# Kernel tuning notes

Measured on AMD Instinct MI355X. Metric: run time of the kernel, lower is better.

## Reference

```python
import jax, jax.numpy as jnp
import numpy as np

NUM_E = 50000
EMBED_DIM = 128
HID_DIM = 200
B = 512
N = 50  # candidate_num / history length
ITER_NUM = 3
ALPHA = 0.5
WEIGHT_BASE = 1.0
SQUASH_W = 1.0
SQUASH_EPS = 1e-9
L2_EPS = 1e-12  # torch F.normalize default eps


def setup_inputs() -> dict:
    key = jax.random.key(0)
    k1, k2, k3, k4, k5, k6, k7 = jax.random.split(key, 7)
    idx = jax.random.randint(k1, (B, N), 0, NUM_E)
    times = jax.random.randint(k2, (B, N), 0, 365)
    # embeddings: normal then row-wise L2 normalize (as in init_embeddings)
    emb = jax.random.normal(k3, (NUM_E, EMBED_DIM), dtype=jnp.float32)
    embeddings = emb / jnp.maximum(jnp.linalg.norm(emb, axis=1, keepdims=True), L2_EPS)
    Ws_w = jax.random.normal(k4, (HID_DIM, EMBED_DIM), dtype=jnp.float32) * (2.0 / (HID_DIM + EMBED_DIM)) ** 0.5
    Ws_b = jnp.zeros((HID_DIM,), dtype=jnp.float32)
    mlp_w = jax.random.normal(k5, (NUM_E, HID_DIM), dtype=jnp.float32) * (2.0 / (NUM_E + HID_DIM)) ** 0.5
    mlp_b = jnp.zeros((NUM_E,), dtype=jnp.float32)
    return {"idx": idx, "times": times, "embeddings": embeddings,
            "Ws_w": Ws_w, "Ws_b": Ws_b, "mlp_w": mlp_w, "mlp_b": mlp_b}


def _squash(s):
    # s: [B, H]; squash over last axis (original axis=-2 on [B,1,1,H,1])
    sq = jnp.sum(s * s, axis=-1, keepdims=True)
    scale = sq / (SQUASH_W + sq) / jnp.sqrt(sq + SQUASH_EPS)
    return scale * s


def reference(idx, times, embeddings, Ws_w, Ws_b, mlp_w, mlp_b):
    # gather history embeddings: [B, N, D]
    embeds = embeddings[idx]
    # temporal weighting -> initial routing logits b_ij: [B, N]
    b = (WEIGHT_BASE + 1.0) / (WEIGHT_BASE + times.astype(jnp.float32))
    # Ws linear (dropout is identity at eval): [B, N, H]
    x = jnp.einsum('bnd,hd->bnh', embeds, Ws_w) + Ws_b
    # u_hat: L2-normalized over H
    u_hat = x / jnp.maximum(jnp.linalg.norm(x, axis=-1, keepdims=True), L2_EPS)
    u_det = jax.lax.stop_gradient(u_hat)
    # dynamic routing, fixed ITER_NUM iterations
    for r in range(ITER_NUM):
        c = jax.nn.softmax(b, axis=1) * N            # [B, N]
        s = jnp.einsum('bn,bnh->bh', c, u_hat)       # [B, H]
        v = _squash(s)                               # [B, H]
        if r < ITER_NUM - 1:
            b = b + jnp.einsum('bnh,bh->bn', u_det, v)
    poses, c_ij = v, c                               # [B, H], [B, N]
    # p_ij: scatter-add c_ij per entity id (math of one_hot^T @ c_ij)
    p = jnp.zeros((B, NUM_E), dtype=jnp.float32)
    p = p.at[jnp.arange(B)[:, None], idx].add(c_ij)
    p = jax.nn.softmax(p, axis=1)
    # decoder mlp (reflect=False)
    scores = poses @ mlp_w.T + mlp_b                 # [B, NUM_E]
    sims = jax.nn.softmax(scores, axis=1)
    return jnp.log(ALPHA * p + (1.0 - ALPHA) * sims)
```

## Files before the change

### kernel.cpp

```cpp
#include <hip/hip_runtime.h>
#include <stdint.h>

#define NUM_E 50000
#define EMBED_DIM 128
#define HID_DIM 200
#define BATCH 512
#define NN 50
#define KPAD 224
#define NKT 7
#define NTT2 3136
#define NXB 196
#define PACK_UNITS 784
#define USTRIDE 201

typedef short s16x8 __attribute__((ext_vector_type(8)));
typedef float f32x4 __attribute__((ext_vector_type(4)));

__device__ inline unsigned short f2bf(float f) {
  union { float f; unsigned u; } v; v.f = f;
  unsigned r = v.u + 0x7FFF + ((v.u >> 16) & 1);
  return (unsigned short)(r >> 16);
}
__device__ inline float bf2f(unsigned short b) {
  union { unsigned u; float f; } v; v.u = ((unsigned)b) << 16;
  return v.f;
}

__device__ __forceinline__ void gl_lds16(const unsigned short* g, unsigned short* l) {
  __builtin_amdgcn_global_load_lds(
      (const __attribute__((address_space(1))) unsigned int*)g,
      (__attribute__((address_space(3))) unsigned int*)l, 16, 0, 0);
}

__global__ __launch_bounds__(256, 4) void k_score(
    const unsigned short* __restrict__ Ap, const unsigned short* __restrict__ Bp,
    const float* __restrict__ mlp_b, unsigned short* __restrict__ stash,
    float* __restrict__ S_ws)
{
  __shared__ __align__(16) char buf[17408];
  const int id = blockIdx.x;
  const int yb = id / 200;
  const int xb = id - yb * 200;
  if (xb >= NXB) return;

  unsigned short* Bs = (unsigned short*)buf;
  float* red = (float*)(buf + 16384);
  const int tid = threadIdx.x;
  const int w = tid >> 6, lane = tid & 63;
  const int q = lane >> 4, l15 = lane & 15;
  const int mt0 = yb * 4;
  const int m0 = yb * 64;
  const int ntb = xb * 16 + w * 4;

  float bias[4];
  #pragma unroll
  for (int nl = 0; nl < 4; ++nl) {
    const int col = (ntb + nl) * 16 + l15;
    bias[nl] = (col < NUM_E) ? mlp_b[col] : 0.f;
  }
  const unsigned short* apBase = Ap + (size_t)mt0 * NKT * 512;

  f32x4 acc[4][4];
  #pragma unroll
  for (int i = 0; i < 4; i++)
    #pragma unroll
    for (int j = 0; j < 4; j++) acc[i][j] = (f32x4){0, 0, 0, 0};

  for (int kt = 0; kt < NKT; ++kt) {
    #pragma unroll
    for (int nl = 0; nl < 4; ++nl)
      gl_lds16(Bp + ((size_t)(ntb + nl) * NKT + kt) * 512 + lane * 8,
               &Bs[(w * 4 + nl) * 512]);
    s16x8 a[4];
    #pragma unroll
    for (int mi = 0; mi < 4; ++mi)
      a[mi] = *(const s16x8*)&apBase[((mi * NKT + kt) * 64 + lane) * 8];
    __syncthreads();
    s16x8 bfr[4];
    #pragma unroll
    for (int nl = 0; nl < 4; ++nl)
      bfr[nl] = *(const s16x8*)&Bs[((w * 4 + nl) * 64 + lane) * 8];
    #pragma unroll
    for (int nl = 0; nl < 4; ++nl)
      #pragma unroll
      for (int mi = 0; mi < 4; ++mi)
        acc[mi][nl] = __builtin_amdgcn_mfma_f32_16x16x32_bf16(a[mi], bfr[nl], acc[mi][nl], 0, 0, 0);
    __syncthreads();
  }

  float rs[4][4];
  #pragma unroll
  for (int mi = 0; mi < 4; mi++)
    #pragma unroll
    for (int p = 0; p < 4; p++) rs[mi][p] = 0.f;
  #pragma unroll
  for (int mi = 0; mi < 4; ++mi)
    #pragma unroll
    for (int nl = 0; nl < 4; ++nl) {
      const int col = (ntb + nl) * 16 + l15;
      #pragma unroll
      for (int p = 0; p < 4; p++) {
        if (col < NUM_E) {
          const float v = acc[mi][nl][p] + bias[nl];
          const unsigned short vb = f2bf(v);
          const int row = m0 + mi * 16 + q * 4 + p;
          stash[(size_t)row * NUM_E + col] = vb;
          rs[mi][p] += __expf(bf2f(vb));
        }
      }
    }
  #pragma unroll
  for (int m = 1; m < 16; m <<= 1)
    for (int mi = 0; mi < 4; mi++)
      for (int p = 0; p < 4; p++)
        rs[mi][p] += __shfl_xor(rs[mi][p], m, 64);
  if (l15 == 0)
    for (int mi = 0; mi < 4; mi++)
      for (int p = 0; p < 4; p++)
        red[w * 64 + mi * 16 + q * 4 + p] = rs[mi][p];
  __syncthreads();
  if (tid < 64)
    atomicAdd(&S_ws[m0 + tid],
              red[tid] + red[64 + tid] + red[128 + tid] + red[192 + tid]);
}

__global__ __launch_bounds__(256) void k_final(
    const unsigned short* __restrict__ stash,
    const float* __restrict__ D_ws, const float* __restrict__ S_ws,
    float* __restrict__ out)
{
  const int COLS8 = NUM_E / 8;
  const int total = BATCH * COLS8;
  const int stride = gridDim.x * 256;
  for (int u = blockIdx.x * 256 + threadIdx.x; u < total; u += stride) {
    const int b = u / COLS8;
    const int c8 = u - b * COLS8;
    const float invD = 0.5f / D_ws[b];
    const float invS = 0.5f / S_ws[b];
    const size_t base = (size_t)b * NUM_E + (size_t)c8 * 8;
    const uint4 raw = *(const uint4*)(stash + base);
    float o[8];
    const unsigned wds[4] = {raw.x, raw.y, raw.z, raw.w};
    #pragma unroll
    for (int j = 0; j < 4; ++j) {
      const float v0 = bf2f((unsigned short)(wds[j] & 0xFFFF));
      const float v1 = bf2f((unsigned short)(wds[j] >> 16));
      o[2 * j]     = __logf(fmaf(__expf(v0), invS, invD));
      o[2 * j + 1] = __logf(fmaf(__expf(v1), invS, invD));
    }
    *(float4*)(out + base)     = make_float4(o[0], o[1], o[2], o[3]);
    *(float4*)(out + base + 4) = make_float4(o[4], o[5], o[6], o[7]);
  }
}

__global__ __launch_bounds__(256, 3) void k_stage1(
    const int* __restrict__ idx, const int* __restrict__ times,
    const float* __restrict__ emb, const float* __restrict__ Ws_w,
    const float* __restrict__ Ws_b, const float* __restrict__ mlp_w,
    unsigned short* __restrict__ Bp, unsigned short* __restrict__ Ap,
    float* __restrict__ poses_f, float* __restrict__ expa_ws,
    float* __restrict__ D_ws, float* __restrict__ S_ws)
{
  __shared__ __align__(16) char buf[40320];
  __shared__ float cc[NN], bb[NN], vv[HID_DIM], red4[4], scaleS;
  __shared__ int sidx[NN];
  const int u = blockIdx.x;
  const int tid = threadIdx.x;
  const int w = tid >> 6, lane = tid & 63;
  const int q = lane >> 4, l15 = lane & 15;

  if (u < BATCH) {
    const int b = u;
    if (tid < NN) {
      sidx[tid] = idx[b * NN + tid];
      bb[tid] = 2.0f / (1.0f + (float)times[b * NN + tid]);
    }
    __syncthreads();
    unsigned short* Afr = (unsigned short*)buf;
    unsigned short* Bfr = (unsigned short*)(buf + 16384);
    for (int v = tid; v < 1024; v += 256) {
      const int row = v >> 4, c = v & 15;
      const int kt = c >> 2, qq = c & 3;
      unsigned short tmp[8] __attribute__((aligned(16)));
      if (row < NN) {
        const float* src = emb + (size_t)sidx[row] * EMBED_DIM + c * 8;
        float4 f0 = *(const float4*)src;
        float4 f1 = *(const float4*)(src + 4);
        tmp[0] = f2bf(f0.x); tmp[1] = f2bf(f0.y); tmp[2] = f2bf(f0.z); tmp[3] = f2bf(f0.w);
        tmp[4] = f2bf(f1.x); tmp[5] = f2bf(f1.y); tmp[6] = f2bf(f1.z); tmp[7] = f2bf(f1.w);
      } else {
        for (int j = 0; j < 8; j++) tmp[j] = 0;
      }
      *(uint4*)&Afr[(((row >> 4) * 4 + kt) * 64 + qq * 16 + (row & 15)) * 8] = *(uint4*)tmp;
    }
    f32x4 acc[4][4];
    #pragma unroll
    for (int i = 0; i < 4; i++)
      #pragma unroll
      for (int j = 0; j < 4; j++) acc[i][j] = (f32x4){0, 0, 0, 0};
    __syncthreads();
    for (int kt = 0; kt < 4; ++kt) {
      for (int v = tid; v < 832; v += 256) {
        const int n = v >> 2, cq = v & 3;
        unsigned short tmp[8] __attribute__((aligned(16)));
        if (n < HID_DIM) {
          const float* src = Ws_w + (size_t)n * EMBED_DIM + kt * 32 + cq * 8;
          float4 f0 = *(const float4*)src;
          float4 f1 = *(const float4*)(src + 4);
          tmp[0] = f2bf(f0.x); tmp[1] = f2bf(f0.y); tmp[2] = f2bf(f0.z); tmp[3] = f2bf(f0.w);
          tmp[4] = f2bf(f1.x); tmp[5] = f2bf(f1.y); tmp[6] = f2bf(f1.z); tmp[7] = f2bf(f1.w);
        } else {
          for (int j = 0; j < 8; j++) tmp[j] = 0;
        }
        *(uint4*)&Bfr[((n >> 4) * 64 + cq * 16 + (n & 15)) * 8] = *(uint4*)tmp;
      }
      __syncthreads();
      s16x8 a[4];
      #pragma unroll
      for (int mt = 0; mt < 4; ++mt)
        a[mt] = *(const s16x8*)&Afr[((mt * 4 + kt) * 64 + lane) * 8];
      #pragma unroll
      for (int ii = 0; ii < 4; ++ii) {
        const int nt = w + ii * 4;
        if (nt < 13) {
          s16x8 bv = *(const s16x8*)&Bfr[(nt * 64 + lane) * 8];
          #pragma unroll
          for (int mt = 0; mt < 4; ++mt)
            acc[mt][ii] = __builtin_amdgcn_mfma_f32_16x16x32_bf16(a[mt], bv, acc[mt][ii], 0, 0, 0);
        }
      }
      __syncthreads();
    }
    float* uu = (float*)buf;
    #pragma unroll
    for (int ii = 0; ii < 4; ++ii) {
      const int nt = w + ii * 4;
      if (nt < 13) {
        const int col = nt * 16 + l15;
        if (col < HID_DIM) {
          const float bv = Ws_b[col];
          #pragma unroll
          for (int mt = 0; mt < 4; ++mt)
            #pragma unroll
            for (int p = 0; p < 4; p++) {
              const int row = mt * 16 + q * 4 + p;
              if (row < NN) uu[row * USTRIDE + col] = acc[mt][ii][p] + bv;
            }
        }
      }
    }
    __syncthreads();
    const int un = tid >> 2, uc0 = (tid & 3) * 50;
    if (un < NN) {
      float s = 0.f;
      for (int j = 0; j < 50; j++) {
        const float x = uu[un * USTRIDE + uc0 + j];
        s += x * x;
      }
      s += __shfl_xor(s, 1, 64);
      s += __shfl_xor(s, 2, 64);
      const float inv = 1.0f / fmaxf(sqrtf(s), 1e-12f);
      for (int j = 0; j < 50; j++) uu[un * USTRIDE + uc0 + j] *= inv;
    }
    __syncthreads();
    for (int it = 0; it < 3; ++it) {
      if (tid < 64) {
        float x = (tid < NN) ? bb[tid] : -1e30f;
        float m = x;
        for (int d = 1; d < 64; d <<= 1) m = fmaxf(m, __shfl_xor(m, d, 64));
        float e = (tid < NN) ? __expf(x - m) : 0.f;
        float s = e;
        for (int d = 1; d < 64; d <<= 1) s += __shfl_xor(s, d, 64);
        if (tid < NN) cc[tid] = e * (float)NN / s;
      }
      __syncthreads();
      float sh = 0.f;
      if (tid < HID_DIM)
        for (int n = 0; n < NN; n++) sh += cc[n] * uu[n * USTRIDE + tid];
      float sq2 = (tid < HID_DIM) ? sh * sh : 0.f;
      for (int d = 1; d < 64; d <<= 1) sq2 += __shfl_xor(sq2, d, 64);
      if ((tid & 63) == 0) red4[tid >> 6] = sq2;
      __syncthreads();
      if (tid == 0) {
        const float t2 = red4[0] + red4[1] + red4[2] + red4[3];
        scaleS = t2 / (1.0f + t2) / sqrtf(t2 + 1e-9f);
      }
      __syncthreads();
      if (tid < HID_DIM) vv[tid] = scaleS * sh;
      __syncthreads();
      if (it < 2) {
        float d = 0.f;
        if (un < NN)
          for (int j = 0; j < 50; j++)
            d += uu[un * USTRIDE + uc0 + j] * vv[uc0 + j];
        d += __shfl_xor(d, 1, 64);
        d += __shfl_xor(d, 2, 64);
        if (un < NN && (tid & 3) == 0) bb[un] += d;
        __syncthreads();
      }
    }
    if (tid < KPAD) {
      const float val = (tid < HID_DIM) ? vv[tid] : 0.f;
      const int kt = tid >> 5, rem = tid & 31, qq = rem >> 3, j = rem & 7;
      const int mt = b >> 4, ll = b & 15;
      Ap[(size_t)(((mt * NKT + kt) * 64) + qq * 16 + ll) * 8 + j] = f2bf(val);
    }
    if (tid < HID_DIM) poses_f[b * HID_DIM + tid] = vv[tid];
    if (tid < 64) {
      float a2 = 0.f; int first = 1;
      const int my = (tid < NN) ? sidx[tid] : -1;
      if (tid < NN) {
        for (int n = 0; n < NN; n++)
          if (sidx[n] == my) { a2 += cc[n]; if (n < tid) first = 0; }
        expa_ws[b * NN + tid] = __expf(a2);
      }
      float contrib = (tid < NN && first) ? (__expf(a2) - 1.0f) : 0.f;
      for (int d = 1; d < 64; d <<= 1) contrib += __shfl_xor(contrib, d, 64);
      if (tid == 0) D_ws[b] = (float)NUM_E + contrib;
    }
  } else if (u < BATCH + PACK_UNITS) {
    const int pb = u - BATCH;
    unsigned short* smem = (unsigned short*)buf;
    const size_t base_f = (size_t)pb * 64 * HID_DIM;
    const float4* src4 = (const float4*)(mlp_w + base_f);
    for (int i = tid; i < 3200; i += 256) {
      float4 f;
      if (base_f + 4 * (size_t)i + 4 <= (size_t)NUM_E * HID_DIM) f = src4[i];
      else f = make_float4(0.f, 0.f, 0.f, 0.f);
      unsigned short t4[4] __attribute__((aligned(8))) = {
        f2bf(f.x), f2bf(f.y), f2bf(f.z), f2bf(f.w)};
      *(uint2*)&smem[i * 4] = *(uint2*)t4;
    }
    __syncthreads();
    const int nt0 = pb * 4;
    unsigned short* dst = Bp + (size_t)nt0 * NKT * 512;
    for (int s2 = 0; s2 < 7; ++s2) {
      const int fi = s2 * 256 + tid;
      const int fr = fi >> 6;
      const int ln = fi & 63;
      const int nt_l = fr / 7, kt = fr - nt_l * 7;
      const int r = nt_l * 16 + (ln & 15);
      const int kb = kt * 32 + (ln >> 4) * 8;
      uint4 val;
      if (kb < HID_DIM) val = *(const uint4*)&smem[r * HID_DIM + kb];
      else val = make_uint4(0, 0, 0, 0);
      *(uint4*)&dst[(size_t)fi * 8] = val;
    }
  } else {
    S_ws[tid] = 0.f;
    S_ws[256 + tid] = 0.f;
  }
}

__global__ __launch_bounds__(256) void k_fix(
    const int* __restrict__ idx, const float* __restrict__ expa,
    const float* __restrict__ poses_f, const float* __restrict__ mlp_w,
    const float* __restrict__ mlp_b, const float* __restrict__ D_ws,
    const float* __restrict__ S_ws, float* __restrict__ out)
{
  const int t = blockIdx.x * 4 + (threadIdx.x >> 6);
  const int lane = threadIdx.x & 63;
  if (t >= BATCH * NN) return;
  const int b = t / NN;
  const int j = idx[t];
  float dot = 0.f;
  for (int h = lane; h < HID_DIM; h += 64)
    dot += poses_f[b * HID_DIM + h] * mlp_w[(size_t)j * HID_DIM + h];
  for (int m = 1; m < 64; m <<= 1) dot += __shfl_xor(dot, m, 64);
  if (lane == 0) {
    const float s = dot + mlp_b[j];
    out[(size_t)b * NUM_E + j] = __logf(0.5f * expa[t] / D_ws[b] +
                                        0.5f * __expf(s) / S_ws[b]);
  }
}

extern "C" void kernel_launch(void* const* d_in, const int* in_sizes, int n_in,
                              void* d_out, int out_size, void* d_ws, size_t ws_size,
                              hipStream_t stream) {
  const int*   idx   = (const int*)d_in[0];
  const int*   times = (const int*)d_in[1];
  const float* emb   = (const float*)d_in[2];
  const float* Ws_w  = (const float*)d_in[3];
  const float* Ws_b  = (const float*)d_in[4];
  const float* mlp_w = (const float*)d_in[5];
  const float* mlp_b = (const float*)d_in[6];
  float* out = (float*)d_out;

  char* ws = (char*)d_ws;
  unsigned short* Bp    = (unsigned short*)ws; ws += (size_t)NTT2 * NKT * 64 * 8 * 2;
  unsigned short* Ap    = (unsigned short*)ws; ws += (size_t)32 * NKT * 64 * 8 * 2;
  float* poses_f        = (float*)ws;          ws += (size_t)BATCH * HID_DIM * 4;
  float* expa           = (float*)ws;          ws += (size_t)BATCH * NN * 4;
  float* D_ws           = (float*)ws;          ws += (size_t)BATCH * 4;
  float* S_ws           = (float*)ws;          ws += (size_t)BATCH * 4;
  unsigned short* stash = (unsigned short*)ws; ws += (size_t)BATCH * NUM_E * 2;

  k_stage1 <<<dim3(BATCH + PACK_UNITS + 1), 256, 0, stream>>>(
      idx, times, emb, Ws_w, Ws_b, mlp_w, Bp, Ap, poses_f, expa, D_ws, S_ws);
  k_score  <<<dim3(1600), 256, 0, stream>>>(Ap, Bp, mlp_b, stash, S_ws);
  k_final  <<<dim3(2048), 256, 0, stream>>>(stash, D_ws, S_ws, out);
  k_fix    <<<dim3(BATCH * NN / 4), 256, 0, stream>>>(idx, expa, poses_f, mlp_w, mlp_b, D_ws, S_ws, out);
}
```

Before: 265.2 us.

## Triple-buffer B tiles and preload A tile into LDS in score GEMM

The score GEMM kernel now stages the whole A tile for the block into LDS up front and streams B k-tiles through a three-deep LDS ring using async global-to-LDS loads two steps ahead. Per-iteration block barriers are replaced by vmcnt waits, since each wave reads only the B slots it loaded itself. This aims to hide global load latency behind MFMA work. It raises LDS use and lowers the occupancy hint from 4 to 2 blocks per CU.

```diff
diff --git a/kernel.cpp b/kernel.cpp
--- a/kernel.cpp
+++ b/kernel.cpp
@@ -32,19 +32,19 @@
       (__attribute__((address_space(3))) unsigned int*)l, 16, 0, 0);
 }
 
-__global__ __launch_bounds__(256, 4) void k_score(
+__global__ __launch_bounds__(256, 2) void k_score(
     const unsigned short* __restrict__ Ap, const unsigned short* __restrict__ Bp,
     const float* __restrict__ mlp_b, unsigned short* __restrict__ stash,
     float* __restrict__ S_ws)
 {
-  __shared__ __align__(16) char buf[17408];
+  __shared__ __align__(16) unsigned short Bs[3][8192];
+  __shared__ __align__(16) unsigned short As[14336];
+  __shared__ float red[256];
   const int id = blockIdx.x;
   const int yb = id / 200;
   const int xb = id - yb * 200;
   if (xb >= NXB) return;
 
-  unsigned short* Bs = (unsigned short*)buf;
-  float* red = (float*)(buf + 16384);
   const int tid = threadIdx.x;
   const int w = tid >> 6, lane = tid & 63;
   const int q = lane >> 4, l15 = lane & 15;
@@ -59,6 +59,21 @@
     bias[nl] = (col < NUM_E) ? mlp_b[col] : 0.f;
   }
   const unsigned short* apBase = Ap + (size_t)mt0 * NKT * 512;
+  const unsigned short* bpB   = Bp + (size_t)ntb * NKT * 512;
+
+  #pragma unroll
+  for (int f = 0; f < 7; ++f) {
+    const int fi = w * 7 + f;
+    gl_lds16(apBase + (size_t)fi * 512 + lane * 8, &As[fi * 512]);
+  }
+  #pragma unroll
+  for (int nl = 0; nl < 4; ++nl)
+    gl_lds16(bpB + (size_t)(nl * NKT + 0) * 512 + lane * 8,
+             &Bs[0][(w * 4 + nl) * 512]);
+  #pragma unroll
+  for (int nl = 0; nl < 4; ++nl)
+    gl_lds16(bpB + (size_t)(nl * NKT + 1) * 512 + lane * 8,
+             &Bs[1][(w * 4 + nl) * 512]);
 
   f32x4 acc[4][4];
   #pragma unroll
@@ -66,26 +81,30 @@
     #pragma unroll
     for (int j = 0; j < 4; j++) acc[i][j] = (f32x4){0, 0, 0, 0};
 
+  __syncthreads();
+
+  #pragma unroll
   for (int kt = 0; kt < NKT; ++kt) {
+    if (kt < NKT - 1) asm volatile("s_waitcnt vmcnt(4)" ::: "memory");
+    else              asm volatile("s_waitcnt vmcnt(0)" ::: "memory");
+    if (kt + 2 < NKT) {
+      #pragma unroll
+      for (int nl = 0; nl < 4; ++nl)
+        gl_lds16(bpB + (size_t)(nl * NKT + kt + 2) * 512 + lane * 8,
+                 &Bs[(kt + 2) % 3][(w * 4 + nl) * 512]);
+    }
+    s16x8 a[4], bfr[4];
+    #pragma unroll
+    for (int mi = 0; mi < 4; ++mi)
+      a[mi] = *(const s16x8*)&As[((mi * NKT + kt) * 64 + lane) * 8];
     #pragma unroll
     for (int nl = 0; nl < 4; ++nl)
-      gl_lds16(Bp + ((size_t)(ntb + nl) * NKT + kt) * 512 + lane * 8,
-               &Bs[(w * 4 + nl) * 512]);
-    s16x8 a[4];
-    #pragma unroll
-    for (int mi = 0; mi < 4; ++mi)
-      a[mi] = *(const s16x8*)&apBase[((mi * NKT + kt) * 64 + lane) * 8];
-    __syncthreads();
-    s16x8 bfr[4];
-    #pragma unroll
-    for (int nl = 0; nl < 4; ++nl)
-      bfr[nl] = *(const s16x8*)&Bs[((w * 4 + nl) * 64 + lane) * 8];
+      bfr[nl] = *(const s16x8*)&Bs[kt % 3][((w * 4 + nl) * 64 + lane) * 8];
     #pragma unroll
     for (int nl = 0; nl < 4; ++nl)
       #pragma unroll
       for (int mi = 0; mi < 4; ++mi)
         acc[mi][nl] = __builtin_amdgcn_mfma_f32_16x16x32_bf16(a[mi], bfr[nl], acc[mi][nl], 0, 0, 0);
-    __syncthreads();
   }
 
   float rs[4][4];
```

Result: no change. 260.7 us (-1.7%).
